# Performance work log

Measured on AMD Instinct MI355X. Metric: run time of the kernel, lower is better.

## Reference

```python
import jax, jax.numpy as jnp
import numpy as np

N = 4096        # num nodes
D = 512         # d_model (in_dim)
F = 512         # dff (out_dim)
H = 4           # num_heads
ALPHA = 0.3     # tf.keras LeakyReLU default


def setup_inputs() -> dict:
    key = jax.random.key(0)
    ks = jax.random.split(key, 9)
    s_in = 1.0 / np.sqrt(D)
    s_out = 1.0 / np.sqrt(F)
    return {
        "nodes": jax.random.normal(ks[0], (N, D), jnp.float32),
        "edges": jax.random.normal(ks[1], (N, D), jnp.float32),
        "labels": jax.random.normal(ks[2], (N, D), jnp.float32),
        # edge_layer Dense(dff)
        "We": jax.random.normal(ks[3], (D, F), jnp.float32) * s_in,
        "be": jnp.zeros((F,), jnp.float32),
        # per-head kernels stacked on leading head axis
        "W": jax.random.normal(ks[4], (H, D, F), jnp.float32) * s_in,
        "b": jax.random.normal(ks[5], (H, F), jnp.float32) * 0.01,
        "u": jax.random.normal(ks[6], (H, F), jnp.float32) * s_out,  # attn_kernel_self (squeezed)
        "v": jax.random.normal(ks[7], (H, F), jnp.float32) * s_out,  # attn_kernel_neighs (squeezed)
    }


def reference(nodes, edges, labels, We, be, W, b, u, v):
    # edge projection shared across heads: Dense(edges + labels)
    e = (edges + labels) @ We + be                       # [N, F]
    # per-head node projection: features = nodes @ W_h + b_h
    feats = jnp.einsum('nd,hdf->hnf', nodes, W) + b[:, None, :]   # [H, N, F]
    # rank-1 additive attention scores
    a_self = jnp.einsum('hnf,hf->hn', feats, u)          # [H, N]
    a_neigh = jnp.einsum('hnf,hf->hn', feats, v)         # [H, N]
    feats = feats + e[None]                              # [H, N, F]
    scores = a_self[:, :, None] * a_neigh[:, None, :]    # [H, N, N] outer product
    scores = jnp.where(scores >= 0, scores, ALPHA * scores)  # LeakyReLU(0.3)
    attn = jax.nn.softmax(scores, axis=-1)               # [H, N, N]
    out = jnp.einsum('hnm,hmf->hnf', attn, feats)        # [H, N, F]
    return jax.nn.relu(out.mean(axis=0))                 # [N, F]
```

## Files before the change

### kernel.cpp

```cpp
#include <hip/hip_runtime.h>

#define NN 4096
#define DD 512
#define FF 512
#define HH 4
#define KK 1024

typedef _Float16 f16;
typedef f16 f16x8 __attribute__((ext_vector_type(8)));
typedef f16 f16x4 __attribute__((ext_vector_type(4)));
typedef float f32x4 __attribute__((ext_vector_type(4)));

typedef __attribute__((address_space(1))) void gvoid;
typedef __attribute__((address_space(3))) void svoid;
__device__ __forceinline__ void glds16(const void* g, void* s) {
    __builtin_amdgcn_global_load_lds((gvoid*)g, (svoid*)s, 16, 0, 0);
}

__device__ __attribute__((aligned(16))) f16 g_catA[NN * KK];
__device__ __attribute__((aligned(16))) f16 g_catB[HH * FF * KK];
__device__ __attribute__((aligned(16))) f16 g_featsH[HH * FF * NN];
__device__ __attribute__((aligned(16))) f16 g_oaccH[(size_t)2 * HH * NN * FF];
__device__ float g_bcat[HH * FF];
__device__ float g_tu[HH * DD], g_tv[HH * DD], g_bu[HH], g_bv[HH];
__device__ float g_p[HH * NN], g_q[HH * NN], g_M[HH * NN], g_sc[HH * NN];

#define PREP_CONV 4104
#define PREP_TRAN 320
#define PREP_UV   513

__global__ __launch_bounds__(256) void k_prep(const float* __restrict__ nodes, const float* __restrict__ edges,
                                              const float* __restrict__ labels, const float* __restrict__ We,
                                              const float* __restrict__ W, const float* __restrict__ be,
                                              const float* __restrict__ b, const float* __restrict__ u,
                                              const float* __restrict__ v) {
    __shared__ float lds[64 * 65];
    int bx = blockIdx.x;
    int tid = threadIdx.x;
    if (bx < PREP_CONV) {
        int id = bx * 256 + tid;
        const int NQ = NN * DD / 4;
        if (id < NQ) {
            f32x4 vv = *(const f32x4*)(nodes + (size_t)id * 4);
            f16x4 ov;
#pragma unroll
            for (int k = 0; k < 4; ++k) ov[k] = (f16)vv[k];
            *(f16x4*)&g_catA[(size_t)(id >> 7) * KK + (id & 127) * 4] = ov;
            return;
        }
        id -= NQ;
        if (id < NQ) {
            f32x4 ev = *(const f32x4*)(edges  + (size_t)id * 4);
            f32x4 lv = *(const f32x4*)(labels + (size_t)id * 4);
            f16x4 ov;
#pragma unroll
            for (int k = 0; k < 4; ++k) ov[k] = (f16)(ev[k] + lv[k]);
            *(f16x4*)&g_catA[(size_t)(id >> 7) * KK + 512 + (id & 127) * 4] = ov;
            return;
        }
        id -= NQ;
        if (id < HH * FF) { g_bcat[id] = b[id] + be[id & 511]; return; }
        return;
    }
    if (bx < PREP_CONV + PREP_TRAN) {
        int bid = bx - PREP_CONV;
        int mi = bid >> 6;
        int t64 = bid & 63;
        const float* src = (mi == 0) ? We : (W + (size_t)(mi - 1) * DD * FF);
        int ti = t64 >> 3, tj = t64 & 7;
        int r = tid >> 2, cseg = (tid & 3) * 16;
#pragma unroll
        for (int kq = 0; kq < 4; ++kq) {
            f32x4 vv = *(const f32x4*)(src + (size_t)(ti * 64 + r) * 512 + tj * 64 + cseg + kq * 4);
            *(f32x4*)&lds[r * 65 + cseg + kq * 4] = vv;
        }
        __syncthreads();
        int fl = tid >> 2, dseg = (tid & 3) * 16;
        f16x8 o0, o1;
#pragma unroll
        for (int k = 0; k < 8; ++k) o0[k] = (f16)lds[(dseg + k) * 65 + fl];
#pragma unroll
        for (int k = 0; k < 8; ++k) o1[k] = (f16)lds[(dseg + 8 + k) * 65 + fl];
        size_t frow = (size_t)(tj * 64 + fl);
        size_t dcol = (size_t)(ti * 64 + dseg);
        if (mi == 0) {
#pragma unroll
            for (int hh = 0; hh < HH; ++hh) {
                size_t ob = ((size_t)hh * FF + frow) * KK + 512 + dcol;
                *(f16x8*)&g_catB[ob] = o0;
                *(f16x8*)&g_catB[ob + 8] = o1;
            }
        } else {
            size_t ob = ((size_t)(mi - 1) * FF + frow) * KK + dcol;
            *(f16x8*)&g_catB[ob] = o0;
            *(f16x8*)&g_catB[ob + 8] = o1;
        }
        return;
    }
    {
        int row = (bx - PREP_CONV - PREP_TRAN) * 4 + (tid >> 6);
        int lane = tid & 63;
        float su = 0.f, sv = 0.f;
        if (row < HH * DD) {
            int h = row >> 9, d = row & 511;
            size_t wb = (size_t)h * DD * FF + (size_t)d * FF;
#pragma unroll
            for (int j = 0; j < 8; ++j) {
                int f = lane + 64 * j;
                float wv = W[wb + f];
                su += wv * u[(size_t)h * FF + f];
                sv += wv * v[(size_t)h * FF + f];
            }
        } else if (row < HH * DD + HH) {
            int h = row - HH * DD;
#pragma unroll
            for (int j = 0; j < 8; ++j) {
                int f = lane + 64 * j;
                float bvv = b[(size_t)h * FF + f];
                su += bvv * u[(size_t)h * FF + f];
                sv += bvv * v[(size_t)h * FF + f];
            }
        }
#pragma unroll
        for (int m = 1; m < 64; m <<= 1) {
            su += __shfl_xor(su, m, 64);
            sv += __shfl_xor(sv, m, 64);
        }
        if (lane == 0 && row < HH * DD + HH) {
            if (row < HH * DD) { g_tu[row] = su; g_tv[row] = sv; }
            else { g_bu[row - HH * DD] = su; g_bv[row - HH * DD] = sv; }
        }
    }
}

__global__ __launch_bounds__(256) void k_pq() {
    int row = blockIdx.x * 4 + (threadIdx.x >> 6);
    int lane = threadIdx.x & 63;
    int h = row >> 12, n = row & 4095;
    const f16* nb = g_catA + (size_t)n * KK + lane * 8;
    const float* tu = g_tu + h * DD + lane * 8;
    const float* tv = g_tv + h * DD + lane * 8;
    f16x8 nv8 = *(const f16x8*)nb;
    f32x4 tu0 = *(const f32x4*)tu, tu1 = *(const f32x4*)(tu + 4);
    f32x4 tv0 = *(const f32x4*)tv, tv1 = *(const f32x4*)(tv + 4);
    float pa = 0.f, qa = 0.f;
#pragma unroll
    for (int j = 0; j < 4; ++j) {
        float nv = (float)nv8[j];
        pa += nv * tu0[j];
        qa += nv * tv0[j];
    }
#pragma unroll
    for (int j = 0; j < 4; ++j) {
        float nv = (float)nv8[4 + j];
        pa += nv * tu1[j];
        qa += nv * tv1[j];
    }
#pragma unroll
    for (int m = 1; m < 64; m <<= 1) {
        pa += __shfl_xor(pa, m, 64);
        qa += __shfl_xor(qa, m, 64);
    }
    if (lane == 0) {
        g_p[row] = pa + g_bu[h];
        g_q[row] = qa + g_bv[h];
    }
}

__global__ __launch_bounds__(256, 2) void k_gemm_feats() {
    __shared__ f16 As[128 * 64];
    __shared__ f16 Bs[128 * 64];
    int tid = threadIdx.x;
    int lane = tid & 63, wave = tid >> 6;
    int wr = wave & 1, wf = wave >> 1;
    int c = lane & 15, g = lane >> 4;
    int n0 = blockIdx.x * 128, f0 = blockIdx.y * 128;
    int h = blockIdx.z;
    const f16* Bgl = g_catB + (size_t)h * FF * KK;
    int r8 = lane >> 3;
    int ksw = ((lane & 7) ^ r8) * 8;
    f32x4 acc[4][4] = {};
    for (int kk = 0; kk < KK; kk += 64) {
        __syncthreads();
#pragma unroll
        for (int j = 0; j < 4; ++j) {
            int row = wave * 32 + j * 8;
            glds16(g_catA + (size_t)(n0 + row + r8) * KK + kk + ksw, &As[row * 64]);
            glds16(Bgl    + (size_t)(f0 + row + r8) * KK + kk + ksw, &Bs[row * 64]);
        }
        __syncthreads();
#pragma unroll
        for (int s = 0; s < 2; ++s) {
            f16x8 af[4], bf[4];
#pragma unroll
            for (int i = 0; i < 4; ++i)
                af[i] = *(const f16x8*)&As[(wr * 64 + i * 16 + c) * 64 + (((s * 4 + g) ^ (c & 7)) * 8)];
#pragma unroll
            for (int jj = 0; jj < 4; ++jj)
                bf[jj] = *(const f16x8*)&Bs[(wf * 64 + jj * 16 + c) * 64 + (((s * 4 + g) ^ (c & 7)) * 8)];
#pragma unroll
            for (int i = 0; i < 4; ++i)
#pragma unroll
                for (int jj = 0; jj < 4; ++jj)
                    acc[i][jj] = __builtin_amdgcn_mfma_f32_16x16x32_f16(af[i], bf[jj], acc[i][jj], 0, 0, 0);
        }
    }
#pragma unroll
    for (int jj = 0; jj < 4; ++jj) {
        int f = f0 + wf * 64 + jj * 16 + c;
        float bv = g_bcat[h * FF + f];
#pragma unroll
        for (int i = 0; i < 4; ++i) {
            int r0 = n0 + wr * 64 + i * 16 + g * 4;
            f16x4 ov;
#pragma unroll
            for (int rr = 0; rr < 4; ++rr) ov[rr] = (f16)(acc[i][jj][rr] + bv);
            *(f16x4*)(g_featsH + ((size_t)h * FF + f) * NN + r0) = ov;
        }
    }
}

__global__ __launch_bounds__(256) void k_msz() {
    __shared__ float qsh[NN];
    __shared__ float red[256];
    int h = blockIdx.y;
    int tid = threadIdx.x;
    float lmax = -1e30f, lmin = 1e30f;
    for (int i = tid; i < NN; i += 256) {
        float qv = g_q[h * NN + i];
        qsh[i] = qv;
        lmax = fmaxf(lmax, qv);
        lmin = fminf(lmin, qv);
    }
    red[tid] = lmax;
    __syncthreads();
    for (int s = 128; s > 0; s >>= 1) {
        if (tid < s) red[tid] = fmaxf(red[tid], red[tid + s]);
        __syncthreads();
    }
    float qmax = red[0];
    __syncthreads();
    red[tid] = lmin;
    __syncthreads();
    for (int s = 128; s > 0; s >>= 1) {
        if (tid < s) red[tid] = fminf(red[tid], red[tid + s]);
        __syncthreads();
    }
    float qmin = red[0];
    __syncthreads();
    int nl = tid & 15, chunk = tid >> 4;
    int n = blockIdx.x * 16 + nl;
    float pv = g_p[h * NN + n];
    float se = pv * (pv >= 0.f ? qmax : qmin);
    float M = fmaxf(se, 0.3f * se);
    float z = 0.f;
    int base = chunk * 256;
    for (int i = 0; i < 64; ++i) {
        f32x4 qv = *(const f32x4*)&qsh[base + i * 4];
#pragma unroll
        for (int k = 0; k < 4; ++k) {
            float s = pv * qv[k];
            s = fmaxf(s, 0.3f * s);
            z += __expf(s - M);
        }
    }
    red[chunk * 16 + nl] = z;
    __syncthreads();
    if (chunk == 0) {
        float Z = 0.f;
#pragma unroll
        for (int t = 0; t < 16; ++t) Z += red[t * 16 + nl];
        g_M[h * NN + n] = M;
        g_sc[h * NN + n] = 0.25f / Z;
    }
}

#define ALD 68
__global__ __launch_bounds__(512, 2) void k_gemm_out() {
    __shared__ f16 As[128 * ALD];
    __shared__ f16 BsL[512 * 32];
    __shared__ f16 BsH[512 * 32];
    int bx = blockIdx.x;
    int grp = bx & 7;
    int h = grp >> 1, ks = grp & 1;
    int n0 = (bx >> 3) * 128;
    int tid = threadIdx.x;
    int lane = tid & 63, wave = tid >> 6;
    int wr = wave & 1;
    int wf = wave >> 1;
    int c = lane & 15, g = lane >> 4;
    int wn = tid >> 2, kq = (tid & 3) * 16;
    float pv = g_p[h * NN + n0 + wn];
    float mv = g_M[h * NN + n0 + wn];
    float sv = g_sc[h * NN + n0 + wn];
    const float* qh = g_q + h * NN + ks * 2048;
    const f16* Bgl = g_featsH + (size_t)h * FF * NN + (size_t)ks * 2048;
    int brow = lane >> 2;
    int bksw = ((lane & 3) ^ (brow & 3)) * 8;
    f32x4 acc[4][8] = {};
    for (int kk = 0; kk < 2048; kk += 64) {
        f16x8 w0, w1;
#pragma unroll
        for (int half = 0; half < 2; ++half) {
            f32x4 qa = *(const f32x4*)(qh + kk + kq + half * 8);
            f32x4 qb = *(const f32x4*)(qh + kk + kq + half * 8 + 4);
#pragma unroll
            for (int k = 0; k < 4; ++k) {
                float s = pv * qa[k];
                s = fmaxf(s, 0.3f * s);
                if (half == 0) w0[k] = (f16)(__expf(s - mv) * sv);
                else           w1[k] = (f16)(__expf(s - mv) * sv);
            }
#pragma unroll
            for (int k = 0; k < 4; ++k) {
                float s = pv * qb[k];
                s = fmaxf(s, 0.3f * s);
                if (half == 0) w0[4 + k] = (f16)(__expf(s - mv) * sv);
                else           w1[4 + k] = (f16)(__expf(s - mv) * sv);
            }
        }
        __syncthreads();
        *(f16x8*)&As[wn * ALD + kq] = w0;
        *(f16x8*)&As[wn * ALD + kq + 8] = w1;
#pragma unroll
        for (int j = 0; j < 4; ++j) {
            int frow = wave * 64 + j * 16;
            glds16(Bgl + (size_t)(frow + brow) * NN + kk + bksw,      &BsL[frow * 32]);
            glds16(Bgl + (size_t)(frow + brow) * NN + kk + 32 + bksw, &BsH[frow * 32]);
        }
        __syncthreads();
#pragma unroll
        for (int s = 0; s < 2; ++s) {
            const f16* Bsrc = (s == 0) ? BsL : BsH;
            f16x8 af[4], bfr[8];
#pragma unroll
            for (int i = 0; i < 4; ++i)
                af[i] = *(const f16x8*)&As[(wr * 64 + i * 16 + c) * ALD + s * 32 + g * 8];
#pragma unroll
            for (int jj = 0; jj < 8; ++jj)
                bfr[jj] = *(const f16x8*)&Bsrc[(wf * 128 + jj * 16 + c) * 32 + ((g ^ (c & 3)) * 8)];
#pragma unroll
            for (int i = 0; i < 4; ++i)
#pragma unroll
                for (int jj = 0; jj < 8; ++jj)
                    acc[i][jj] = __builtin_amdgcn_mfma_f32_16x16x32_f16(af[i], bfr[jj], acc[i][jj], 0, 0, 0);
        }
    }
    f16* O = g_oaccH + (size_t)grp * NN * FF;
#pragma unroll
    for (int jj = 0; jj < 8; ++jj) {
        int f = wf * 128 + jj * 16 + c;
#pragma unroll
        for (int i = 0; i < 4; ++i) {
            int r0 = n0 + wr * 64 + i * 16 + g * 4;
#pragma unroll
            for (int rr = 0; rr < 4; ++rr)
                O[(size_t)(r0 + rr) * FF + f] = (f16)acc[i][jj][rr];
        }
    }
}

__global__ void k_reduce(float* __restrict__ out) {
    size_t i = ((size_t)blockIdx.x * 256 + threadIdx.x) * 4;
    const size_t NF = (size_t)NN * FF;
    f32x4 s = {0.f, 0.f, 0.f, 0.f};
#pragma unroll
    for (int sl = 0; sl < 8; ++sl) {
        f16x4 v = *(const f16x4*)(g_oaccH + sl * NF + i);
#pragma unroll
        for (int rr = 0; rr < 4; ++rr) s[rr] += (float)v[rr];
    }
    f32x4 o;
#pragma unroll
    for (int rr = 0; rr < 4; ++rr) o[rr] = fmaxf(s[rr], 0.f);
    *(f32x4*)(out + i) = o;
}

extern "C" void kernel_launch(void* const* d_in, const int* in_sizes, int n_in,
                              void* d_out, int out_size, void* d_ws, size_t ws_size,
                              hipStream_t stream) {
    (void)in_sizes; (void)n_in; (void)out_size; (void)d_ws; (void)ws_size;
    const float* nodes  = (const float*)d_in[0];
    const float* edges  = (const float*)d_in[1];
    const float* labels = (const float*)d_in[2];
    const float* We     = (const float*)d_in[3];
    const float* be     = (const float*)d_in[4];
    const float* W      = (const float*)d_in[5];
    const float* b      = (const float*)d_in[6];
    const float* u      = (const float*)d_in[7];
    const float* v      = (const float*)d_in[8];

    k_prep<<<PREP_CONV + PREP_TRAN + PREP_UV, 256, 0, stream>>>(nodes, edges, labels, We, W, be, b, u, v);
    k_pq<<<4096, 256, 0, stream>>>();
    k_gemm_feats<<<dim3(32, 4, 4), 256, 0, stream>>>();
    k_msz<<<dim3(256, 4), 256, 0, stream>>>();
    k_gemm_out<<<256, 512, 0, stream>>>();
    k_reduce<<<2048, 256, 0, stream>>>((float*)d_out);
}
```

Baseline: 268.1 us.

## Fuse softmax denominator into output GEMM and widen feats GEMM K-tile

Removes the separate pass that computed the softmax normaliser over all N×N scores. The output GEMM now accumulates unnormalised exponentials (scaled by a constant) and writes per-split partial sums. The reduce kernel applies 0.25/Z per head during the final sum. A tiny kernel now computes only the row max bound. The feats GEMM also doubles its K tile to 128 with a new XOR swizzle, halving the number of sync rounds. The block order of the output GEMM changes from interleaved heads to a 3D grid, which may affect cache locality. Unnormalised f16 weights and f16 partial outputs risk precision loss.

```diff
diff --git a/kernel.cpp b/kernel.cpp
--- a/kernel.cpp
+++ b/kernel.cpp
@@ -21,9 +21,10 @@
 __device__ __attribute__((aligned(16))) f16 g_catB[HH * FF * KK];
 __device__ __attribute__((aligned(16))) f16 g_featsH[HH * FF * NN];
 __device__ __attribute__((aligned(16))) f16 g_oaccH[(size_t)2 * HH * NN * FF];
+__device__ float g_Zp[2 * HH * NN];
 __device__ float g_bcat[HH * FF];
 __device__ float g_tu[HH * DD], g_tv[HH * DD], g_bu[HH], g_bv[HH];
-__device__ float g_p[HH * NN], g_q[HH * NN], g_M[HH * NN], g_sc[HH * NN];
+__device__ float g_p[HH * NN], g_q[HH * NN], g_M[HH * NN];
 
 #define PREP_CONV 4104
 #define PREP_TRAN 320
@@ -168,36 +169,42 @@
 }
 
 __global__ __launch_bounds__(256, 2) void k_gemm_feats() {
-    __shared__ f16 As[128 * 64];
-    __shared__ f16 Bs[128 * 64];
+    __shared__ f16 As[128 * 128];
+    __shared__ f16 Bs[128 * 128];
     int tid = threadIdx.x;
     int lane = tid & 63, wave = tid >> 6;
-    int wr = wave & 1, wf = wave >> 1;
+    int wr = wave & 1, wc = wave >> 1;
     int c = lane & 15, g = lane >> 4;
     int n0 = blockIdx.x * 128, f0 = blockIdx.y * 128;
     int h = blockIdx.z;
     const f16* Bgl = g_catB + (size_t)h * FF * KK;
-    int r8 = lane >> 3;
-    int ksw = ((lane & 7) ^ r8) * 8;
+    int r4 = lane >> 4;
+    int ch = lane & 15;
     f32x4 acc[4][4] = {};
-    for (int kk = 0; kk < KK; kk += 64) {
-        __syncthreads();
-#pragma unroll
-        for (int j = 0; j < 4; ++j) {
-            int row = wave * 32 + j * 8;
-            glds16(g_catA + (size_t)(n0 + row + r8) * KK + kk + ksw, &As[row * 64]);
-            glds16(Bgl    + (size_t)(f0 + row + r8) * KK + kk + ksw, &Bs[row * 64]);
-        }
-        __syncthreads();
-#pragma unroll
-        for (int s = 0; s < 2; ++s) {
+    for (int kk = 0; kk < KK; kk += 128) {
+        __syncthreads();
+#pragma unroll
+        for (int j = 0; j < 8; ++j) {
+            int rowb = wave * 32 + j * 4;
+            int row = rowb + r4;
+            int src = (ch ^ (row & 15)) * 8;
+            glds16(g_catA + (size_t)(n0 + row) * KK + kk + src, &As[rowb * 128]);
+            glds16(Bgl    + (size_t)(f0 + row) * KK + kk + src, &Bs[rowb * 128]);
+        }
+        __syncthreads();
+#pragma unroll
+        for (int s = 0; s < 4; ++s) {
             f16x8 af[4], bf[4];
 #pragma unroll
-            for (int i = 0; i < 4; ++i)
-                af[i] = *(const f16x8*)&As[(wr * 64 + i * 16 + c) * 64 + (((s * 4 + g) ^ (c & 7)) * 8)];
-#pragma unroll
-            for (int jj = 0; jj < 4; ++jj)
-                bf[jj] = *(const f16x8*)&Bs[(wf * 64 + jj * 16 + c) * 64 + (((s * 4 + g) ^ (c & 7)) * 8)];
+            for (int i = 0; i < 4; ++i) {
+                int ra = wr * 64 + i * 16 + c;
+                af[i] = *(const f16x8*)&As[ra * 128 + (((s * 4 + g) ^ (ra & 15)) * 8)];
+            }
+#pragma unroll
+            for (int jj = 0; jj < 4; ++jj) {
+                int rb = wc * 64 + jj * 16 + c;
+                bf[jj] = *(const f16x8*)&Bs[rb * 128 + (((s * 4 + g) ^ (rb & 15)) * 8)];
+            }
 #pragma unroll
             for (int i = 0; i < 4; ++i)
 #pragma unroll
@@ -207,7 +214,7 @@
     }
 #pragma unroll
     for (int jj = 0; jj < 4; ++jj) {
-        int f = f0 + wf * 64 + jj * 16 + c;
+        int f = f0 + wc * 64 + jj * 16 + c;
         float bv = g_bcat[h * FF + f];
 #pragma unroll
         for (int i = 0; i < 4; ++i) {
@@ -220,15 +227,13 @@
     }
 }
 
-__global__ __launch_bounds__(256) void k_msz() {
-    __shared__ float qsh[NN];
+__global__ __launch_bounds__(256) void k_mstat() {
     __shared__ float red[256];
-    int h = blockIdx.y;
+    int h = blockIdx.x;
     int tid = threadIdx.x;
     float lmax = -1e30f, lmin = 1e30f;
     for (int i = tid; i < NN; i += 256) {
         float qv = g_q[h * NN + i];
-        qsh[i] = qv;
         lmax = fmaxf(lmax, qv);
         lmin = fminf(lmin, qv);
     }
@@ -247,31 +252,12 @@
         __syncthreads();
     }
     float qmin = red[0];
-    __syncthreads();
-    int nl = tid & 15, chunk = tid >> 4;
-    int n = blockIdx.x * 16 + nl;
-    float pv = g_p[h * NN + n];
-    float se = pv * (pv >= 0.f ? qmax : qmin);
-    float M = fmaxf(se, 0.3f * se);
-    float z = 0.f;
-    int base = chunk * 256;
-    for (int i = 0; i < 64; ++i) {
-        f32x4 qv = *(const f32x4*)&qsh[base + i * 4];
-#pragma unroll
-        for (int k = 0; k < 4; ++k) {
-            float s = pv * qv[k];
-            s = fmaxf(s, 0.3f * s);
-            z += __expf(s - M);
-        }
-    }
-    red[chunk * 16 + nl] = z;
-    __syncthreads();
-    if (chunk == 0) {
-        float Z = 0.f;
-#pragma unroll
-        for (int t = 0; t < 16; ++t) Z += red[t * 16 + nl];
-        g_M[h * NN + n] = M;
-        g_sc[h * NN + n] = 0.25f / Z;
+#pragma unroll
+    for (int j = 0; j < 16; ++j) {
+        int n = tid + j * 256;
+        float pv = g_p[h * NN + n];
+        float se = pv * (pv >= 0.f ? qmax : qmin);
+        g_M[h * NN + n] = fmaxf(se, 0.3f * se);
     }
 }
 
@@ -280,23 +266,23 @@
     __shared__ f16 As[128 * ALD];
     __shared__ f16 BsL[512 * 32];
     __shared__ f16 BsH[512 * 32];
-    int bx = blockIdx.x;
-    int grp = bx & 7;
-    int h = grp >> 1, ks = grp & 1;
-    int n0 = (bx >> 3) * 128;
     int tid = threadIdx.x;
     int lane = tid & 63, wave = tid >> 6;
     int wr = wave & 1;
     int wf = wave >> 1;
     int c = lane & 15, g = lane >> 4;
+    int n0 = blockIdx.x * 128;
+    int h = blockIdx.y;
+    int ks = blockIdx.z;
     int wn = tid >> 2, kq = (tid & 3) * 16;
+    const float C = 0.015625f;
     float pv = g_p[h * NN + n0 + wn];
     float mv = g_M[h * NN + n0 + wn];
-    float sv = g_sc[h * NN + n0 + wn];
     const float* qh = g_q + h * NN + ks * 2048;
     const f16* Bgl = g_featsH + (size_t)h * FF * NN + (size_t)ks * 2048;
     int brow = lane >> 2;
     int bksw = ((lane & 3) ^ (brow & 3)) * 8;
+    float zacc = 0.f;
     f32x4 acc[4][8] = {};
     for (int kk = 0; kk < 2048; kk += 64) {
         f16x8 w0, w1;
@@ -308,15 +294,19 @@
             for (int k = 0; k < 4; ++k) {
                 float s = pv * qa[k];
                 s = fmaxf(s, 0.3f * s);
-                if (half == 0) w0[k] = (f16)(__expf(s - mv) * sv);
-                else           w1[k] = (f16)(__expf(s - mv) * sv);
+                float e = __expf(s - mv) * C;
+                zacc += e;
+                if (half == 0) w0[k] = (f16)e;
+                else           w1[k] = (f16)e;
             }
 #pragma unroll
             for (int k = 0; k < 4; ++k) {
                 float s = pv * qb[k];
                 s = fmaxf(s, 0.3f * s);
-                if (half == 0) w0[4 + k] = (f16)(__expf(s - mv) * sv);
-                else           w1[4 + k] = (f16)(__expf(s - mv) * sv);
+                float e = __expf(s - mv) * C;
+                zacc += e;
+                if (half == 0) w0[4 + k] = (f16)e;
+                else           w1[4 + k] = (f16)e;
             }
         }
         __syncthreads();
@@ -346,7 +336,10 @@
                     acc[i][jj] = __builtin_amdgcn_mfma_f32_16x16x32_f16(af[i], bfr[jj], acc[i][jj], 0, 0, 0);
         }
     }
-    f16* O = g_oaccH + (size_t)grp * NN * FF;
+    zacc += __shfl_xor(zacc, 1, 64);
+    zacc += __shfl_xor(zacc, 2, 64);
+    if ((tid & 3) == 0) g_Zp[(size_t)(h * 2 + ks) * NN + n0 + wn] = zacc;
+    f16* O = g_oaccH + (size_t)(h * 2 + ks) * NN * FF;
 #pragma unroll
     for (int jj = 0; jj < 8; ++jj) {
         int f = wf * 128 + jj * 16 + c;
@@ -361,14 +354,19 @@
 }
 
 __global__ void k_reduce(float* __restrict__ out) {
-    size_t i = ((size_t)blockIdx.x * 256 + threadIdx.x) * 4;
+    int t = blockIdx.x * 256 + threadIdx.x;
+    size_t i = (size_t)t * 4;
+    int n = t >> 7;
     const size_t NF = (size_t)NN * FF;
     f32x4 s = {0.f, 0.f, 0.f, 0.f};
 #pragma unroll
-    for (int sl = 0; sl < 8; ++sl) {
-        f16x4 v = *(const f16x4*)(g_oaccH + sl * NF + i);
-#pragma unroll
-        for (int rr = 0; rr < 4; ++rr) s[rr] += (float)v[rr];
+    for (int h = 0; h < HH; ++h) {
+        float Z = g_Zp[(size_t)(2 * h) * NN + n] + g_Zp[(size_t)(2 * h + 1) * NN + n];
+        float sc = 0.25f / Z;
+        f16x4 a = *(const f16x4*)(g_oaccH + (size_t)(2 * h) * NF + i);
+        f16x4 bsl = *(const f16x4*)(g_oaccH + (size_t)(2 * h + 1) * NF + i);
+#pragma unroll
+        for (int rr = 0; rr < 4; ++rr) s[rr] += ((float)a[rr] + (float)bsl[rr]) * sc;
     }
     f32x4 o;
 #pragma unroll
@@ -393,7 +391,7 @@
     k_prep<<<PREP_CONV + PREP_TRAN + PREP_UV, 256, 0, stream>>>(nodes, edges, labels, We, W, be, b, u, v);
     k_pq<<<4096, 256, 0, stream>>>();
     k_gemm_feats<<<dim3(32, 4, 4), 256, 0, stream>>>();
-    k_msz<<<dim3(256, 4), 256, 0, stream>>>();
-    k_gemm_out<<<256, 512, 0, stream>>>();
+    k_mstat<<<HH, 256, 0, stream>>>();
+    k_gemm_out<<<dim3(32, 4, 2), 512, 0, stream>>>();
     k_reduce<<<2048, 256, 0, stream>>>((float*)d_out);
 }
```

New measurement: 247.7 us. 7.6% less time.
